# Optimization experiments

Hardware: AMD Instinct MI355X
Metric: run time of the kernel (lower is better)

Reference implementation:

```python
import jax, jax.numpy as jnp
import numpy as np

B, C, H, W, R = 8, 256, 64, 64, 16


def setup_inputs() -> dict:
    key = jax.random.key(0)
    ks = jax.random.split(key, 14)
    def w(k, shape, fan):
        return (jax.random.normal(k, shape, jnp.float32) / np.sqrt(fan)).astype(jnp.float32)
    return {
        "features_depth": jax.random.normal(ks[0], (B, C, H, W), jnp.float32),
        "features_semseg": jax.random.normal(ks[1], (B, C, H, W), jnp.float32),
        "W0": w(ks[2], (C, 2 * C), 2 * C),          # conv_split0 1x1, [out,in]
        "Wdw": w(ks[3], (C, 1, 3, 3), 9),            # depthwise 3x3, groups=C
        "Wq": w(ks[4], (C, C), C),                   # Linear weights [out,in]
        "Wk": w(ks[5], (C, C), C),
        "Wv": w(ks[6], (C, C), C),
        "Wp": w(ks[7], (C, C), C),
        "bp": jnp.zeros((C,), jnp.float32),
        "Wsplit": w(ks[8], (C, C), C),               # conv_split 1x1
        "se_d_w1": w(ks[9], (C // R, C), C),         # SE squeeze conv1x1 (depth)
        "se_d_w2": w(ks[10], (C, C // R), C // R),
        "se_s_w1": w(ks[11], (C // R, C), C),        # SE squeeze conv1x1 (semseg)
        "se_s_w2": w(ks[12], (C, C // R), C // R),
    }


def _l2norm(a, eps=1e-12):
    n = jnp.linalg.norm(a, axis=-1, keepdims=True)
    return a / jnp.maximum(n, eps)


def _se(x, w1, w2):
    # x: [B,C,H,W]; global avg pool -> 1x1 convs -> sigmoid gate
    p = x.mean(axis=(2, 3))                                  # [B,C]
    h = jax.nn.relu(jnp.einsum('rc,bc->br', w1, p))          # [B,C/R]
    g = jax.nn.sigmoid(jnp.einsum('cr,br->bc', w2, h))       # [B,C]
    return x * g[:, :, None, None]


def reference(features_depth, features_semseg, W0, Wdw, Wq, Wk, Wv, Wp, bp,
              Wsplit, se_d_w1, se_d_w2, se_s_w1, se_s_w2):
    x = jnp.concatenate([features_depth, features_semseg], axis=1)  # [B,2C,H,W]
    x = jnp.einsum('oc,bchw->bohw', W0, x)                          # 1x1 conv
    x = jax.lax.conv_general_dilated(
        x, Wdw, window_strides=(1, 1), padding='SAME',
        dimension_numbers=('NCHW', 'OIHW', 'NCHW'), feature_group_count=C)
    xt = x.transpose(0, 2, 3, 1).reshape(B, H * W, C)               # [B,N,C]
    q = (xt @ Wq.T).transpose(0, 2, 1)                              # [B,C,N]
    k = (xt @ Wk.T).transpose(0, 2, 1)
    v = (xt @ Wv.T).transpose(0, 2, 1)
    q = _l2norm(q)
    k = _l2norm(k)
    attn = jax.nn.softmax(jnp.einsum('bcn,bdn->bcd', k, q), axis=-1)  # [B,C,C]
    y = jnp.einsum('bcd,bdn->bcn', attn, v)                         # [B,C,N]
    y = y.transpose(0, 2, 1)                                        # [B,N,C]
    y = y @ Wp.T + bp                                               # proj
    out_c = y.reshape(B, H, W, C).transpose(0, 3, 1, 2)             # [B,C,H,W]
    out_c = jnp.einsum('oc,bchw->bohw', Wsplit, out_c)              # 1x1 conv
    out_depth = _se(out_c, se_d_w1, se_d_w2) + features_depth
    out_semseg = _se(out_c, se_s_w1, se_s_w2) + features_semseg
    return (out_depth, out_semseg)
```

## Files before the change

kernel.cpp:

```cpp
#include <hip/hip_runtime.h>
#include <cstdint>

#define DEVI __device__ __forceinline__

using fx4 = __attribute__((ext_vector_type(4))) float;
using bf8 = __attribute__((ext_vector_type(8))) __bf16;
using s8v = __attribute__((ext_vector_type(8))) short;
typedef unsigned short u16;
typedef unsigned int u32;

DEVI float b2f(u16 u) { return __builtin_bit_cast(float, (u32)u << 16); }
DEVI u16 f2b(float f) {
  u32 u = __builtin_bit_cast(u32, f);
  return (u16)((u + 0x7fffu + ((u >> 16) & 1u)) >> 16);
}

#define GLOAD(g, l)                                                          \
  __builtin_amdgcn_global_load_lds(                                          \
      (const __attribute__((address_space(1))) unsigned int*)(g),            \
      (__attribute__((address_space(3))) unsigned int*)(l), 16, 0, 0)

__global__ __launch_bounds__(256) void wcvt(const float* s0, u16* d0, int n0,
                                            const float* s1, u16* d1, int n1,
                                            const float* s2, u16* d2, int n2,
                                            const float* s3, u16* d3, int n3) {
  const float* s; u16* d; int n;
  switch (blockIdx.y) {
    case 0: s = s0; d = d0; n = n0; break;
    case 1: s = s1; d = d1; n = n1; break;
    case 2: s = s2; d = d2; n = n2; break;
    default: s = s3; d = d3; n = n3; break;
  }
  int i = blockIdx.x * 256 + threadIdx.x;
  if (i < n) d[i] = f2b(s[i]);
}

__global__ __launch_bounds__(256) void wcmul(const float* __restrict__ Wsp,
                                             const float* __restrict__ Wp,
                                             const float* __restrict__ bp,
                                             u16* __restrict__ wcb, float* __restrict__ bc) {
  const int o = blockIdx.x, t = threadIdx.x;
  __shared__ float row[256];
  __shared__ float red[4];
  row[t] = Wsp[o * 256 + t];
  __syncthreads();
  float acc = 0.f;
  for (int c = 0; c < 256; ++c) acc += row[c] * Wp[c * 256 + t];
  wcb[o * 256 + t] = f2b(acc);
  float pb = row[t] * bp[t];
#pragma unroll
  for (int m = 32; m > 0; m >>= 1) pb += __shfl_xor(pb, m);
  if ((t & 63) == 0) red[t >> 6] = pb;
  __syncthreads();
  if (t == 0) bc[o] = red[0] + red[1] + red[2] + red[3];
}

__global__ void pack_cat(const float* __restrict__ fd, const float* __restrict__ fs,
                         u16* __restrict__ out) {
  __shared__ float t[32][33];
  const int b = blockIdx.z;
  const int n0 = blockIdx.x * 32;
  const int g = blockIdx.y;
  const float* src = (g < 8) ? fd : fs;
  const int c0 = (g & 7) * 32;
  const int ccol0 = g * 32;
  const int tx = threadIdx.x;
  const int ty = threadIdx.y;
  const float* sp = src + ((long)b * 256 + c0) * 4096 + n0;
#pragma unroll
  for (int i = 0; i < 4; ++i) {
    int c = ty + i * 8;
    t[c][tx] = sp[(long)c * 4096 + tx];
  }
  __syncthreads();
  u16* op = out + ((long)b * 4096 + n0) * 512 + ccol0;
#pragma unroll
  for (int i = 0; i < 4; ++i) {
    int r = ty + i * 8;
    op[(long)r * 512 + tx] = f2b(t[tx][r]);
  }
}

template <typename OT, int BIAS, bool POOL>
__global__ __launch_bounds__(256) void gemm_nt(
    const u16* __restrict__ A, long sA, int lda,
    const u16* __restrict__ B, long sB, int ldb,
    OT* __restrict__ C, long sC, long sCs, int ldc,
    const float* __restrict__ bias, int Keff, int ksplit,
    float* __restrict__ poolpart) {
  __shared__ u16 ldsA[128 * 64];
  __shared__ u16 ldsB[128 * 64];
  const int z = blockIdx.z;
  const int bb = z / ksplit;
  const int ss = z - bb * ksplit;
  const int bm = blockIdx.x * 128;
  const int bn = blockIdx.y * 128;
  const u16* Ab = A + bb * sA + (long)ss * Keff + (long)bm * lda;
  const u16* Bb = B + bb * sB + (long)ss * Keff + (long)bn * ldb;
  const int tid = threadIdx.x;
  const int wid = tid >> 6;
  const int lane = tid & 63;
  const int wm = wid >> 1, wn = wid & 1;
  const int srow = tid >> 3;
  const int slot = tid & 7;

  fx4 acc[4][4] = {};
  for (int kt = 0; kt < Keff; kt += 64) {
#pragma unroll
    for (int i = 0; i < 4; ++i) {
      const int row = i * 32 + srow;
      const int kq = slot ^ (row & 7);
      GLOAD(Ab + (long)row * lda + kt + kq * 8, &ldsA[i * 2048 + wid * 512]);
      GLOAD(Bb + (long)row * ldb + kt + kq * 8, &ldsB[i * 2048 + wid * 512]);
    }
    __syncthreads();
#pragma unroll
    for (int ko = 0; ko < 2; ++ko) {
      bf8 af[4], bfr[4];
      const int kq = ko * 4 + (lane >> 4);
#pragma unroll
      for (int f = 0; f < 4; ++f) {
        const int ar = wm * 64 + f * 16 + (lane & 15);
        af[f] = *(const bf8*)&ldsA[ar * 64 + ((kq ^ (ar & 7)) * 8)];
        const int br = wn * 64 + f * 16 + (lane & 15);
        bfr[f] = *(const bf8*)&ldsB[br * 64 + ((kq ^ (br & 7)) * 8)];
      }
#pragma unroll
      for (int fm = 0; fm < 4; ++fm)
#pragma unroll
        for (int fn = 0; fn < 4; ++fn)
          acc[fm][fn] = __builtin_amdgcn_mfma_f32_16x16x32_bf16(af[fm], bfr[fn], acc[fm][fn], 0, 0, 0);
    }
    __syncthreads();
  }
  OT* Cb = C + bb * sC + ss * sCs;
  float pr[4][4];
  if (POOL) {
#pragma unroll
    for (int fm = 0; fm < 4; ++fm)
#pragma unroll
      for (int r = 0; r < 4; ++r) pr[fm][r] = 0.f;
  }
#pragma unroll
  for (int fm = 0; fm < 4; ++fm) {
    const int m0 = bm + wm * 64 + fm * 16 + ((lane >> 4) << 2);
#pragma unroll
    for (int fn = 0; fn < 4; ++fn) {
      const int n0 = bn + wn * 64 + fn * 16 + (lane & 15);
      float bvn = (BIAS == 1) ? bias[n0] : 0.f;
#pragma unroll
      for (int r = 0; r < 4; ++r) {
        float v = acc[fm][fn][r] + bvn;
        if (BIAS == 2) v += bias[m0 + r];
        if constexpr (sizeof(OT) == 2) Cb[(long)(m0 + r) * ldc + n0] = (OT)f2b(v);
        else Cb[(long)(m0 + r) * ldc + n0] = v;
        if (POOL) pr[fm][r] += v;
      }
    }
  }
  if (POOL) {
#pragma unroll
    for (int fm = 0; fm < 4; ++fm)
#pragma unroll
      for (int r = 0; r < 4; ++r) {
        float s = pr[fm][r];
        s += __shfl_xor(s, 1); s += __shfl_xor(s, 2);
        s += __shfl_xor(s, 4); s += __shfl_xor(s, 8);
        if ((lane & 15) == 0) {
          const int o = bm + wm * 64 + fm * 16 + ((lane >> 4) << 2) + r;
          poolpart[(long)(blockIdx.y * 2 + wn) * 2048 + bb * 256 + o] = s;
        }
      }
  }
}

__global__ __launch_bounds__(256) void dwconv3x3(const u16* __restrict__ x,
                                                 const float* __restrict__ wdw,
                                                 u16* __restrict__ y) {
  __shared__ float w[9][256];
  const int t = threadIdx.x;
  for (int i = t; i < 2304; i += 256) w[i % 9][i / 9] = wdw[i];
  __syncthreads();
  const int nb = blockIdx.x;
  const int b = nb >> 9;
  const int n0 = (nb & 511) << 3;
  const int tn = t >> 5;
  const int tc = (t & 31) << 3;
  const int n = n0 + tn;
  const int hh = n >> 6, ww2 = n & 63;
  const u16* base = x + ((long)b << 20);
  float acc[8] = {0.f, 0.f, 0.f, 0.f, 0.f, 0.f, 0.f, 0.f};
#pragma unroll
  for (int ky = 0; ky < 3; ++ky) {
    const int hy = hh + ky - 1;
    if ((unsigned)hy >= 64u) continue;
#pragma unroll
    for (int kx = 0; kx < 3; ++kx) {
      const int wx = ww2 + kx - 1;
      if ((unsigned)wx >= 64u) continue;
      const s8v v = *(const s8v*)&base[(((hy << 6) + wx) << 8) + tc];
      const int kk = ky * 3 + kx;
      const fx4 wa = *(const fx4*)&w[kk][tc];
      const fx4 wb = *(const fx4*)&w[kk][tc + 4];
#pragma unroll
      for (int j = 0; j < 4; ++j) {
        acc[j] += wa[j] * b2f((u16)v[j]);
        acc[4 + j] += wb[j] * b2f((u16)v[4 + j]);
      }
    }
  }
  s8v o;
#pragma unroll
  for (int j = 0; j < 8; ++j) o[j] = (short)f2b(acc[j]);
  *(s8v*)&y[((long)b << 20) + ((long)n << 8) + tc] = o;
}

__global__ __launch_bounds__(256) void rownorm(const u16* __restrict__ qk,
                                               float* __restrict__ rinv) {
  const long row = blockIdx.x;
  const u16* p = qk + row * 4096;
  const int t = threadIdx.x;
  float ss = 0.f;
#pragma unroll
  for (int c = 0; c < 2; ++c) {
    s8v a = ((const s8v*)p)[t * 2 + c];
#pragma unroll
    for (int j = 0; j < 8; ++j) { float x = b2f((u16)a[j]); ss += x * x; }
  }
#pragma unroll
  for (int o = 32; o > 0; o >>= 1) ss += __shfl_xor(ss, o);
  __shared__ float red[4];
  if ((t & 63) == 0) red[t >> 6] = ss;
  __syncthreads();
  if (t == 0) rinv[row] = 1.f / fmaxf(sqrtf(red[0] + red[1] + red[2] + red[3]), 1e-12f);
}

__global__ __launch_bounds__(256) void softmax_splits(const float* __restrict__ part,
                                                      const float* __restrict__ rinv,
                                                      u16* __restrict__ out) {
  const int wid = threadIdx.x >> 6, lane = threadIdx.x & 63;
  const long row = (long)blockIdx.x * 4 + wid;
  const int b = (int)(row >> 8);
  const int c = (int)(row & 255);
  fx4 v = {0.f, 0.f, 0.f, 0.f};
#pragma unroll
  for (int s = 0; s < 8; ++s)
    v += ((const fx4*)(part + s * 524288 + row * 256))[lane];
  const float rk = rinv[b * 512 + 256 + c];
  const fx4 rq = *(const fx4*)&rinv[b * 512 + lane * 4];
  v[0] *= rk * rq[0]; v[1] *= rk * rq[1]; v[2] *= rk * rq[2]; v[3] *= rk * rq[3];
  float m = fmaxf(fmaxf(v[0], v[1]), fmaxf(v[2], v[3]));
#pragma unroll
  for (int o = 32; o > 0; o >>= 1) m = fmaxf(m, __shfl_xor(m, o));
  float e0 = __expf(v[0] - m), e1 = __expf(v[1] - m);
  float e2 = __expf(v[2] - m), e3 = __expf(v[3] - m);
  float s4 = e0 + e1 + e2 + e3;
#pragma unroll
  for (int o = 32; o > 0; o >>= 1) s4 += __shfl_xor(s4, o);
  const float inv = 1.f / s4;
  u16* op = out + row * 256 + lane * 4;
  op[0] = f2b(e0 * inv); op[1] = f2b(e1 * inv);
  op[2] = f2b(e2 * inv); op[3] = f2b(e3 * inv);
}

__global__ __launch_bounds__(256) void se_gates(const float* __restrict__ poolpart,
                                                const float* __restrict__ w1d, const float* __restrict__ w2d,
                                                const float* __restrict__ w1s, const float* __restrict__ w2s,
                                                float* __restrict__ gd, float* __restrict__ gs) {
  const int b = blockIdx.x;
  const int t = threadIdx.x;
  __shared__ float p[256], hd[16], hs[16];
  float s = 0.f;
#pragma unroll 8
  for (int sl = 0; sl < 64; ++sl) s += poolpart[(long)sl * 2048 + b * 256 + t];
  p[t] = s * (1.f / 4096.f);
  __syncthreads();
  if (t < 16) {
    float ad = 0.f, as2 = 0.f;
    for (int j = 0; j < 256; ++j) {
      ad += w1d[t * 256 + j] * p[j];
      as2 += w1s[t * 256 + j] * p[j];
    }
    hd[t] = fmaxf(ad, 0.f);
    hs[t] = fmaxf(as2, 0.f);
  }
  __syncthreads();
  float ad = 0.f, as2 = 0.f;
#pragma unroll
  for (int r = 0; r < 16; ++r) {
    ad += w2d[t * 16 + r] * hd[r];
    as2 += w2s[t * 16 + r] * hs[r];
  }
  gd[b * 256 + t] = 1.f / (1.f + __expf(-ad));
  gs[b * 256 + t] = 1.f / (1.f + __expf(-as2));
}

__global__ __launch_bounds__(256) void fuse_out(const u16* __restrict__ oc,
                                                const float* __restrict__ gd, const float* __restrict__ gs,
                                                const float* __restrict__ fd, const float* __restrict__ fs,
                                                float* __restrict__ od, float* __restrict__ os) {
  const long i = ((long)blockIdx.x * 256 + threadIdx.x) * 8;
  const long bc = i >> 12;
  const float gdv = gd[bc], gsv = gs[bc];
  const s8v c8 = *(const s8v*)&oc[i];
  const fx4 a0 = *(const fx4*)(fd + i), a1 = *(const fx4*)(fd + i + 4);
  const fx4 s0 = *(const fx4*)(fs + i), s1 = *(const fx4*)(fs + i + 4);
  fx4 d0, d1, e0, e1;
#pragma unroll
  for (int j = 0; j < 4; ++j) {
    const float cl = b2f((u16)c8[j]);
    const float ch = b2f((u16)c8[4 + j]);
    d0[j] = cl * gdv + a0[j]; d1[j] = ch * gdv + a1[j];
    e0[j] = cl * gsv + s0[j]; e1[j] = ch * gsv + s1[j];
  }
  *(fx4*)(od + i) = d0; *(fx4*)(od + i + 4) = d1;
  *(fx4*)(os + i) = e0; *(fx4*)(os + i + 4) = e1;
}

extern "C" void kernel_launch(void* const* d_in, const int* in_sizes, int n_in,
                              void* d_out, int out_size, void* d_ws, size_t ws_size,
                              hipStream_t stream) {
  const float* fd  = (const float*)d_in[0];
  const float* fs  = (const float*)d_in[1];
  const float* W0  = (const float*)d_in[2];
  const float* Wdw = (const float*)d_in[3];
  const float* Wq  = (const float*)d_in[4];
  const float* Wk  = (const float*)d_in[5];
  const float* Wv  = (const float*)d_in[6];
  const float* Wp  = (const float*)d_in[7];
  const float* bp  = (const float*)d_in[8];
  const float* Wsp = (const float*)d_in[9];
  const float* w1d = (const float*)d_in[10];
  const float* w2d = (const float*)d_in[11];
  const float* w1s = (const float*)d_in[12];
  const float* w2s = (const float*)d_in[13];

  char* ws = (char*)d_ws;
  u16* catb   = (u16*)(ws + 0);
  u16* qkb    = catb;
  u16* x0b    = (u16*)(ws + 33554432);
  u16* ytb    = x0b;
  u16* xtb    = (u16*)(ws + 50331648);
  u16* outcb  = xtb;
  u16* vtb    = (u16*)(ws + 67108864);
  u16* asmb   = (u16*)(ws + 83886080);
  float* part = (float*)(ws + 84934656);
  u16* w0b    = (u16*)(ws + 101711872);
  u16* wqkb   = (u16*)(ws + 101974016);
  u16* wvb    = (u16*)(ws + 102236160);
  u16* wcb    = (u16*)(ws + 102367232);
  float* bcb  = (float*)(ws + 102498304);
  float* rinv = (float*)(ws + 102499328);
  float* poolpart = (float*)(ws + 102515712);
  float* gdp  = (float*)(ws + 103040000);
  float* gsp  = (float*)(ws + 103048192);
  float* od  = (float*)d_out;
  float* osg = od + 8388608;

  wcvt<<<dim3(512, 4), 256, 0, stream>>>(W0, w0b, 131072, Wq, wqkb, 65536,
                                         Wk, wqkb + 65536, 65536, Wv, wvb, 65536);
  wcmul<<<256, 256, 0, stream>>>(Wsp, Wp, bp, wcb, bcb);
  pack_cat<<<dim3(128, 16, 8), dim3(32, 8), 0, stream>>>(fd, fs, catb);
  gemm_nt<u16, 0, false><<<dim3(32, 2, 8), 256, 0, stream>>>(
      catb, 2097152, 512, w0b, 0, 512, x0b, 1048576, 0, 256, nullptr, 512, 1, nullptr);
  dwconv3x3<<<4096, 256, 0, stream>>>(x0b, Wdw, xtb);
  gemm_nt<u16, 0, false><<<dim3(4, 32, 8), 256, 0, stream>>>(
      wqkb, 0, 256, xtb, 1048576, 256, qkb, 2097152, 0, 4096, nullptr, 256, 1, nullptr);
  gemm_nt<u16, 0, false><<<dim3(32, 2, 8), 256, 0, stream>>>(
      xtb, 1048576, 256, wvb, 0, 256, vtb, 1048576, 0, 256, nullptr, 256, 1, nullptr);
  rownorm<<<4096, 256, 0, stream>>>(qkb, rinv);
  gemm_nt<float, 0, false><<<dim3(2, 2, 64), 256, 0, stream>>>(
      qkb + 1048576, 2097152, 4096, qkb, 2097152, 4096,
      part, 65536, 524288, 256, nullptr, 512, 8, nullptr);
  softmax_splits<<<512, 256, 0, stream>>>(part, rinv, asmb);
  gemm_nt<u16, 0, false><<<dim3(32, 2, 8), 256, 0, stream>>>(
      vtb, 1048576, 256, asmb, 65536, 256, ytb, 1048576, 0, 256, nullptr, 256, 1, nullptr);
  gemm_nt<u16, 2, true><<<dim3(2, 32, 8), 256, 0, stream>>>(
      wcb, 0, 256, ytb, 1048576, 256, outcb, 1048576, 0, 4096, bcb, 256, 1, poolpart);
  se_gates<<<8, 256, 0, stream>>>(poolpart, w1d, w2d, w1s, w2s, gdp, gsp);
  fuse_out<<<4096, 256, 0, stream>>>(outcb, gdp, gsp, fd, fs, od, osg);
}
```

Baseline: 179.4 us.

## Reassociate channel attention through the Gram matrix of the conv output

```diff
diff --git a/kernel.cpp b/kernel.cpp
--- a/kernel.cpp
+++ b/kernel.cpp
@@ -6,6 +6,7 @@
 using fx4 = __attribute__((ext_vector_type(4))) float;
 using bf8 = __attribute__((ext_vector_type(8))) __bf16;
 using s8v = __attribute__((ext_vector_type(8))) short;
+using s4v = __attribute__((ext_vector_type(4))) short;
 typedef unsigned short u16;
 typedef unsigned int u32;
 
@@ -20,19 +21,28 @@
       (const __attribute__((address_space(1))) unsigned int*)(g),            \
       (__attribute__((address_space(3))) unsigned int*)(l), 16, 0, 0)
 
-__global__ __launch_bounds__(256) void wcvt(const float* s0, u16* d0, int n0,
-                                            const float* s1, u16* d1, int n1,
-                                            const float* s2, u16* d2, int n2,
-                                            const float* s3, u16* d3, int n3) {
-  const float* s; u16* d; int n;
-  switch (blockIdx.y) {
-    case 0: s = s0; d = d0; n = n0; break;
-    case 1: s = s1; d = d1; n = n1; break;
-    case 2: s = s2; d = d2; n = n2; break;
-    default: s = s3; d = d3; n = n3; break;
-  }
-  int i = blockIdx.x * 256 + threadIdx.x;
-  if (i < n) d[i] = f2b(s[i]);
+__global__ __launch_bounds__(256) void prep(const float* __restrict__ W0,
+                                            const float* __restrict__ Wq,
+                                            const float* __restrict__ Wk,
+                                            const float* __restrict__ Wv,
+                                            u16* __restrict__ w0b,
+                                            u16* __restrict__ wqk2,
+                                            u16* __restrict__ wvtb) {
+  const int i = blockIdx.x * 256 + threadIdx.x;
+  if (blockIdx.y == 0) {
+    if (i < 131072) w0b[i] = f2b(W0[i]);
+  } else if (blockIdx.y == 1) {
+    if (i < 524288) {
+      const int row = i >> 9, c = i & 511;
+      const float* src = (row < 256) ? Wq : Wk;
+      wqk2[i] = f2b(src[((row & 255) << 8) + (c & 255)]);
+    }
+  } else {
+    if (i < 65536) {
+      const int e = i >> 8, d = i & 255;
+      wvtb[i] = f2b(Wv[d * 256 + e]);
+    }
+  }
 }
 
 __global__ __launch_bounds__(256) void wcmul(const float* __restrict__ Wsp,
@@ -147,10 +157,9 @@
 #pragma unroll
     for (int fn = 0; fn < 4; ++fn) {
       const int n0 = bn + wn * 64 + fn * 16 + (lane & 15);
-      float bvn = (BIAS == 1) ? bias[n0] : 0.f;
 #pragma unroll
       for (int r = 0; r < 4; ++r) {
-        float v = acc[fm][fn][r] + bvn;
+        float v = acc[fm][fn][r];
         if (BIAS == 2) v += bias[m0 + r];
         if constexpr (sizeof(OT) == 2) Cb[(long)(m0 + r) * ldc + n0] = (OT)f2b(v);
         else Cb[(long)(m0 + r) * ldc + n0] = v;
@@ -215,37 +224,85 @@
   *(s8v*)&y[((long)b << 20) + ((long)n << 8) + tc] = o;
 }
 
-__global__ __launch_bounds__(256) void rownorm(const u16* __restrict__ qk,
-                                               float* __restrict__ rinv) {
-  const long row = blockIdx.x;
-  const u16* p = qk + row * 4096;
-  const int t = threadIdx.x;
-  float ss = 0.f;
-#pragma unroll
-  for (int c = 0; c < 2; ++c) {
-    s8v a = ((const s8v*)p)[t * 2 + c];
-#pragma unroll
-    for (int j = 0; j < 8; ++j) { float x = b2f((u16)a[j]); ss += x * x; }
-  }
-#pragma unroll
-  for (int o = 32; o > 0; o >>= 1) ss += __shfl_xor(ss, o);
-  __shared__ float red[4];
-  if ((t & 63) == 0) red[t >> 6] = ss;
-  __syncthreads();
-  if (t == 0) rinv[row] = 1.f / fmaxf(sqrtf(red[0] + red[1] + red[2] + red[3]), 1e-12f);
-}
-
-__global__ __launch_bounds__(256) void softmax_splits(const float* __restrict__ part,
-                                                      const float* __restrict__ rinv,
-                                                      u16* __restrict__ out) {
+__global__ void btrans(const u16* __restrict__ x, u16* __restrict__ y) {
+  __shared__ u16 t[32][34];
+  const int b = blockIdx.z;
+  const int n0 = blockIdx.x * 32;
+  const int c0 = blockIdx.y * 32;
+  const int tx = threadIdx.x, ty = threadIdx.y;
+  const u16* sp = x + (long)b * 1048576 + (long)n0 * 256 + c0;
+#pragma unroll
+  for (int j = 0; j < 4; ++j) {
+    int i = ty + j * 8;
+    t[i][tx] = sp[(long)i * 256 + tx];
+  }
+  __syncthreads();
+  u16* op = y + (long)b * 1048576 + (long)c0 * 4096 + n0;
+#pragma unroll
+  for (int j = 0; j < 4; ++j) {
+    int r = ty + j * 8;
+    op[(long)r * 4096 + tx] = t[tx][r];
+  }
+}
+
+__global__ __launch_bounds__(256) void gsplit(const float* __restrict__ part,
+                                              u16* __restrict__ G2) {
+  const int i4 = (blockIdx.x * 256 + threadIdx.x) * 4;
+  fx4 s = {0.f, 0.f, 0.f, 0.f};
+#pragma unroll
+  for (int ss = 0; ss < 8; ++ss) s += *(const fx4*)(part + (long)ss * 524288 + i4);
+  const int b = i4 >> 16, rem = i4 & 65535, e = rem >> 8, c0 = rem & 255;
+  u16* d = G2 + (long)b * 131072 + (long)e * 512 + c0;
+  s4v hi, lo;
+#pragma unroll
+  for (int j = 0; j < 4; ++j) {
+    u16 h = f2b(s[j]);
+    hi[j] = (short)h;
+    lo[j] = (short)f2b(s[j] - b2f(h));
+  }
+  *(s4v*)d = hi;
+  *(s4v*)(d + 256) = lo;
+}
+
+__global__ __launch_bounds__(256) void ssplit_diag(const float* __restrict__ SS,
+                                                   const float* __restrict__ Wq,
+                                                   const float* __restrict__ Wk,
+                                                   u16* __restrict__ S2,
+                                                   float* __restrict__ rinv) {
+  const int wid = threadIdx.x >> 6, lane = threadIdx.x & 63;
+  const int gid = blockIdx.x * 4 + wid;
+  const int b = gid >> 9, row = gid & 511;
+  const float* ssrow = SS + (long)b * 131072 + (long)row * 256;
+  const float* wrow = (row < 256) ? (Wq + row * 256) : (Wk + (row - 256) * 256);
+  const fx4 sv = ((const fx4*)ssrow)[lane];
+  const fx4 wv = ((const fx4*)wrow)[lane];
+  float dot = sv[0] * wv[0] + sv[1] * wv[1] + sv[2] * wv[2] + sv[3] * wv[3];
+#pragma unroll
+  for (int o = 32; o > 0; o >>= 1) dot += __shfl_xor(dot, o);
+  if (lane == 0)
+    rinv[b * 512 + row] = 1.f / fmaxf(sqrtf(fmaxf(dot, 0.f)), 1e-12f);
+  if (row < 256) {
+    u16* d = S2 + (long)b * 131072 + (long)row * 512 + lane * 4;
+    s4v hi, lo;
+#pragma unroll
+    for (int j = 0; j < 4; ++j) {
+      u16 h = f2b(sv[j]);
+      hi[j] = (short)h;
+      lo[j] = (short)f2b(sv[j] - b2f(h));
+    }
+    *(s4v*)d = hi;
+    *(s4v*)(d + 256) = lo;
+  }
+}
+
+__global__ __launch_bounds__(256) void softmax_g(const float* __restrict__ araw,
+                                                 const float* __restrict__ rinv,
+                                                 u16* __restrict__ out) {
   const int wid = threadIdx.x >> 6, lane = threadIdx.x & 63;
   const long row = (long)blockIdx.x * 4 + wid;
   const int b = (int)(row >> 8);
   const int c = (int)(row & 255);
-  fx4 v = {0.f, 0.f, 0.f, 0.f};
-#pragma unroll
-  for (int s = 0; s < 8; ++s)
-    v += ((const fx4*)(part + s * 524288 + row * 256))[lane];
+  fx4 v = ((const fx4*)(araw + row * 256))[lane];
   const float rk = rinv[b * 512 + 256 + c];
   const fx4 rq = *(const fx4*)&rinv[b * 512 + lane * 4];
   v[0] *= rk * rq[0]; v[1] *= rk * rq[1]; v[2] *= rk * rq[2]; v[3] *= rk * rq[3];
@@ -337,46 +394,53 @@
 
   char* ws = (char*)d_ws;
   u16* catb   = (u16*)(ws + 0);
-  u16* qkb    = catb;
+  u16* xtT    = (u16*)(ws + 0);
   u16* x0b    = (u16*)(ws + 33554432);
-  u16* ytb    = x0b;
+  u16* outcb  = x0b;
   u16* xtb    = (u16*)(ws + 50331648);
-  u16* outcb  = xtb;
-  u16* vtb    = (u16*)(ws + 67108864);
-  u16* asmb   = (u16*)(ws + 83886080);
-  float* part = (float*)(ws + 84934656);
-  u16* w0b    = (u16*)(ws + 101711872);
-  u16* wqkb   = (u16*)(ws + 101974016);
-  u16* wvb    = (u16*)(ws + 102236160);
-  u16* wcb    = (u16*)(ws + 102367232);
-  float* bcb  = (float*)(ws + 102498304);
-  float* rinv = (float*)(ws + 102499328);
-  float* poolpart = (float*)(ws + 102515712);
-  float* gdp  = (float*)(ws + 103040000);
-  float* gsp  = (float*)(ws + 103048192);
+  float* part = (float*)(ws + 67108864);
+  u16* G2     = (u16*)(ws + 83886080);
+  float* SS   = (float*)(ws + 85983232);
+  u16* S2     = (u16*)(ws + 90177536);
+  float* araw = (float*)(ws + 92274688);
+  u16* attnb  = (u16*)(ws + 94371840);
+  u16* m1t    = (u16*)(ws + 95420416);
+  u16* wfin   = (u16*)(ws + 96468992);
+  u16* w0b    = (u16*)(ws + 97517568);
+  u16* wqk2   = (u16*)(ws + 97779712);
+  u16* wvtb   = (u16*)(ws + 98304000);
+  u16* wcb    = (u16*)(ws + 98435072);
+  float* bcb  = (float*)(ws + 98566144);
+  float* rinv = (float*)(ws + 98567168);
+  float* poolpart = (float*)(ws + 98583552);
+  float* gdp  = (float*)(ws + 99108864);
+  float* gsp  = (float*)(ws + 99117056);
   float* od  = (float*)d_out;
   float* osg = od + 8388608;
 
-  wcvt<<<dim3(512, 4), 256, 0, stream>>>(W0, w0b, 131072, Wq, wqkb, 65536,
-                                         Wk, wqkb + 65536, 65536, Wv, wvb, 65536);
+  prep<<<dim3(2048, 3), 256, 0, stream>>>(W0, Wq, Wk, Wv, w0b, wqk2, wvtb);
   wcmul<<<256, 256, 0, stream>>>(Wsp, Wp, bp, wcb, bcb);
   pack_cat<<<dim3(128, 16, 8), dim3(32, 8), 0, stream>>>(fd, fs, catb);
   gemm_nt<u16, 0, false><<<dim3(32, 2, 8), 256, 0, stream>>>(
       catb, 2097152, 512, w0b, 0, 512, x0b, 1048576, 0, 256, nullptr, 512, 1, nullptr);
   dwconv3x3<<<4096, 256, 0, stream>>>(x0b, Wdw, xtb);
-  gemm_nt<u16, 0, false><<<dim3(4, 32, 8), 256, 0, stream>>>(
-      wqkb, 0, 256, xtb, 1048576, 256, qkb, 2097152, 0, 4096, nullptr, 256, 1, nullptr);
-  gemm_nt<u16, 0, false><<<dim3(32, 2, 8), 256, 0, stream>>>(
-      xtb, 1048576, 256, wvb, 0, 256, vtb, 1048576, 0, 256, nullptr, 256, 1, nullptr);
-  rownorm<<<4096, 256, 0, stream>>>(qkb, rinv);
+  btrans<<<dim3(128, 8, 8), dim3(32, 8), 0, stream>>>(xtb, xtT);
   gemm_nt<float, 0, false><<<dim3(2, 2, 64), 256, 0, stream>>>(
-      qkb + 1048576, 2097152, 4096, qkb, 2097152, 4096,
+      xtT, 1048576, 4096, xtT, 1048576, 4096,
       part, 65536, 524288, 256, nullptr, 512, 8, nullptr);
-  softmax_splits<<<512, 256, 0, stream>>>(part, rinv, asmb);
-  gemm_nt<u16, 0, false><<<dim3(32, 2, 8), 256, 0, stream>>>(
-      vtb, 1048576, 256, asmb, 65536, 256, ytb, 1048576, 0, 256, nullptr, 256, 1, nullptr);
+  gsplit<<<512, 256, 0, stream>>>(part, G2);
+  gemm_nt<float, 0, false><<<dim3(4, 2, 8), 256, 0, stream>>>(
+      wqk2, 0, 512, G2, 131072, 512, SS, 131072, 0, 256, nullptr, 512, 1, nullptr);
+  ssplit_diag<<<1024, 256, 0, stream>>>(SS, Wq, Wk, S2, rinv);
+  gemm_nt<float, 0, false><<<dim3(2, 2, 8), 256, 0, stream>>>(
+      wqk2 + 131072, 0, 512, S2, 131072, 512, araw, 65536, 0, 256, nullptr, 512, 1, nullptr);
+  softmax_g<<<512, 256, 0, stream>>>(araw, rinv, attnb);
+  gemm_nt<u16, 0, false><<<dim3(2, 2, 8), 256, 0, stream>>>(
+      wvtb, 0, 256, attnb, 65536, 256, m1t, 65536, 0, 256, nullptr, 256, 1, nullptr);
+  gemm_nt<u16, 0, false><<<dim3(2, 2, 8), 256, 0, stream>>>(
+      wcb, 0, 256, m1t, 65536, 256, wfin, 65536, 0, 256, nullptr, 256, 1, nullptr);
   gemm_nt<u16, 2, true><<<dim3(2, 32, 8), 256, 0, stream>>>(
-      wcb, 0, 256, ytb, 1048576, 256, outcb, 1048576, 0, 4096, bcb, 256, 1, poolpart);
+      wfin, 65536, 256, xtb, 1048576, 256, outcb, 1048576, 0, 4096, bcb, 256, 1, poolpart);
   se_gates<<<8, 256, 0, stream>>>(poolpart, w1d, w2d, w1s, w2s, gdp, gsp);
   fuse_out<<<4096, 256, 0, stream>>>(outcb, gdp, gsp, fd, fs, od, osg);
 }
```

Result: slower. 183.9 us (+2.5%).
